# Kernel optimization log

Measured on AMD Instinct MI355X. Metric: run time of the kernel, lower is better.

The kernel has to match this reference:

```python
import jax, jax.numpy as jnp
import numpy as np

SEQ, BATCH, IN_DIM, HID_DIM = 512, 256, 256, 256
NQ = 8
ALPHA = 0.5
MLP_HID = 128


def _linear_init(key, fan_in, fan_out):
    k1, k2 = jax.random.split(key)
    bound = 1.0 / np.sqrt(fan_in)
    W = jax.random.uniform(k1, (fan_in, fan_out), minval=-bound, maxval=bound, dtype=jnp.float32)
    b = jax.random.uniform(k2, (fan_out,), minval=-bound, maxval=bound, dtype=jnp.float32)
    return W, b


def setup_inputs() -> dict:
    key = jax.random.key(0)
    ks = jax.random.split(key, 12)
    cdim = IN_DIM + HID_DIM
    inputs = jax.random.normal(ks[0], (SEQ, BATCH, IN_DIM), dtype=jnp.float32)
    W1, b1 = _linear_init(ks[1], cdim, MLP_HID)
    W2, b2 = _linear_init(ks[2], MLP_HID, NQ * 4)
    Wf, bf = _linear_init(ks[3], cdim, 1)
    Wi, bi = _linear_init(ks[4], cdim, 1)
    Wg, bg = _linear_init(ks[5], cdim, 1)
    Wo, bo = _linear_init(ks[6], cdim, 1)
    rzf = jax.random.normal(ks[7], (NQ,), dtype=jnp.float32)
    rzi = jax.random.normal(ks[8], (NQ,), dtype=jnp.float32)
    rzg = jax.random.normal(ks[9], (NQ,), dtype=jnp.float32)
    rzo = jax.random.normal(ks[10], (NQ,), dtype=jnp.float32)
    return dict(inputs=inputs, W1=W1, b1=b1, W2=W2, b2=b2,
                Wf=Wf, bf=bf, Wi=Wi, bi=bi, Wg=Wg, bg=bg, Wo=Wo, bo=bo,
                rzf=rzf, rzi=rzi, rzg=rzg, rzo=rzo)


def _qgate(theta):
    # Analytic expectations of the RX/RZ/CNOT-chain circuit:
    # <Z_k> = prod_{j<=k} cos(theta_j); rz_params cancel in Z expectations.
    # Returns mean over wires, shape (batch, 1).
    return jnp.mean(jnp.cumprod(jnp.cos(theta), axis=-1), axis=-1, keepdims=True)


def reference(inputs, W1, b1, W2, b2, Wf, bf, Wi, bi, Wg, bg, Wo, bo, rzf, rzi, rzg, rzo):
    batch = inputs.shape[1]
    hx0 = jnp.zeros((batch, HID_DIM), dtype=inputs.dtype)
    cx0 = jnp.zeros((batch, HID_DIM), dtype=inputs.dtype)

    def step(carry, x):
        hx, cx = carry
        combined = jnp.concatenate([x, hx], axis=1)  # (B, in+hid)
        f_c = jax.nn.sigmoid(combined @ Wf + bf)
        i_c = jax.nn.sigmoid(combined @ Wi + bi)
        g_c = jnp.tanh(combined @ Wg + bg)
        o_c = jax.nn.sigmoid(combined @ Wo + bo)
        h1 = jax.nn.relu(combined @ W1 + b1)
        q = h1 @ W2 + b2  # (B, 4*NQ)
        q_f = _qgate(q[:, 0 * NQ:1 * NQ])
        q_i = _qgate(q[:, 1 * NQ:2 * NQ])
        q_g = _qgate(q[:, 2 * NQ:3 * NQ])
        q_o = _qgate(q[:, 3 * NQ:4 * NQ])
        f = (1 - ALPHA) * f_c + ALPHA * jax.nn.sigmoid(q_f)
        i = (1 - ALPHA) * i_c + ALPHA * jax.nn.sigmoid(q_i)
        g = (1 - ALPHA) * g_c + ALPHA * jnp.tanh(q_g)
        o = (1 - ALPHA) * o_c + ALPHA * jax.nn.sigmoid(q_o)
        cx_new = f * cx + i * g
        hx_new = o * jnp.tanh(cx_new)
        return (hx_new, cx_new), hx_new

    (hx, cx), outputs = jax.lax.scan(step, (hx0, cx0), inputs)
    return outputs, (hx, cx)
```

## Files before the change

kernel.cpp:

```cpp
#include <hip/hip_runtime.h>

#define SEQ 512
#define BATCH 256
#define INDIM 256
#define MLP 128
#define M_ROWS (SEQ * BATCH)
#define PRE_STRIDE 136
#define AUX_OFF ((size_t)M_ROWS * PRE_STRIDE)

__global__ __launch_bounds__(256) void prep_kernel(
    const float* __restrict__ W1,
    const float* __restrict__ Wf, const float* __restrict__ Wi,
    const float* __restrict__ Wg, const float* __restrict__ Wo,
    const float* __restrict__ bf, const float* __restrict__ bi,
    const float* __restrict__ bg, const float* __restrict__ bo,
    float* __restrict__ aux) {
  const int tid = threadIdx.x;
  if (tid < 128) {
    float s = 0.f;
    for (int k = 0; k < 256; ++k) s += W1[(size_t)(256 + k) * 128 + tid];
    aux[tid] = s;
  } else if (tid < 132) {
    const int g = tid - 128;
    const float* w = (g == 0) ? Wf : (g == 1) ? Wi : (g == 2) ? Wg : Wo;
    float s = 0.f;
    for (int k = 0; k < 256; ++k) s += w[256 + k];
    aux[128 + g] = s;
  } else if (tid < 136) {
    const int g = tid - 132;
    const float* bp = (g == 0) ? bf : (g == 1) ? bi : (g == 2) ? bg : bo;
    aux[132 + g] = bp[0];
  }
}

#define BK 16
#define LDX 132

__global__ __launch_bounds__(256) void gemm_kernel(
    const float* __restrict__ X,
    const float* __restrict__ W1,
    const float* __restrict__ b1p,
    const float* __restrict__ Wf, const float* __restrict__ Wi,
    const float* __restrict__ Wg, const float* __restrict__ Wo,
    const float* __restrict__ bfp, const float* __restrict__ bip,
    const float* __restrict__ bgp, const float* __restrict__ bop,
    float* __restrict__ PRE) {
  __shared__ __align__(16) float Xs[BK * LDX];
  __shared__ __align__(16) float Ws[BK * LDX];
  __shared__ float Wgs[BK * 4];

  const int tid = threadIdx.x;
  const int blk = blockIdx.x;
  const int tx = tid & 15, ty = tid >> 4;
  const int r_st = tid >> 1, kh = (tid & 1) * 8;
  const int wk = tid >> 4, wn = (tid & 15) * 8;
  const int r2 = tid >> 1, gp = (tid & 1) * 2;

  const size_t rowbase = (size_t)blk * 128;

  float acc[8][8] = {};
  float ga = 0.f, gb = 0.f;

  for (int kc = 0; kc < 256; kc += BK) {
    const float4 xa = *(const float4*)&X[(rowbase + r_st) * 256 + kc + kh];
    const float4 xb = *(const float4*)&X[(rowbase + r_st) * 256 + kc + kh + 4];
    const float4 wa = *(const float4*)&W1[(size_t)(kc + wk) * 128 + wn];
    const float4 wb = *(const float4*)&W1[(size_t)(kc + wk) * 128 + wn + 4];
    float wgv = 0.f;
    if (tid < 64) {
      const int kk = tid >> 2, g = tid & 3;
      const float* w = (g == 0) ? Wf : (g == 1) ? Wi : (g == 2) ? Wg : Wo;
      wgv = w[kc + kk];
    }
    __syncthreads();
    Xs[(kh + 0) * LDX + r_st] = xa.x;
    Xs[(kh + 1) * LDX + r_st] = xa.y;
    Xs[(kh + 2) * LDX + r_st] = xa.z;
    Xs[(kh + 3) * LDX + r_st] = xa.w;
    Xs[(kh + 4) * LDX + r_st] = xb.x;
    Xs[(kh + 5) * LDX + r_st] = xb.y;
    Xs[(kh + 6) * LDX + r_st] = xb.z;
    Xs[(kh + 7) * LDX + r_st] = xb.w;
    *(float4*)&Ws[wk * LDX + wn] = wa;
    *(float4*)&Ws[wk * LDX + wn + 4] = wb;
    if (tid < 64) Wgs[tid] = wgv;
    __syncthreads();

#pragma unroll
    for (int kk = 0; kk < BK; ++kk) {
      const float4 a0 = *(const float4*)&Xs[kk * LDX + ty * 8];
      const float4 a1 = *(const float4*)&Xs[kk * LDX + ty * 8 + 4];
      const float4 c0 = *(const float4*)&Ws[kk * LDX + tx * 8];
      const float4 c1 = *(const float4*)&Ws[kk * LDX + tx * 8 + 4];
      const float av[8] = {a0.x, a0.y, a0.z, a0.w, a1.x, a1.y, a1.z, a1.w};
      const float bv[8] = {c0.x, c0.y, c0.z, c0.w, c1.x, c1.y, c1.z, c1.w};
#pragma unroll
      for (int i = 0; i < 8; ++i)
#pragma unroll
        for (int j = 0; j < 8; ++j)
          acc[i][j] = fmaf(av[i], bv[j], acc[i][j]);
      const float xv = Xs[kk * LDX + r2];
      ga = fmaf(xv, Wgs[kk * 4 + gp], ga);
      gb = fmaf(xv, Wgs[kk * 4 + gp + 1], gb);
    }
  }

  float bias[8];
  {
    const float4 u0 = *(const float4*)&b1p[tx * 8];
    const float4 u1 = *(const float4*)&b1p[tx * 8 + 4];
    bias[0] = u0.x; bias[1] = u0.y; bias[2] = u0.z; bias[3] = u0.w;
    bias[4] = u1.x; bias[5] = u1.y; bias[6] = u1.z; bias[7] = u1.w;
  }
#pragma unroll
  for (int i = 0; i < 8; ++i) {
    const size_t row = rowbase + ty * 8 + i;
    float4 o0, o1;
    o0.x = acc[i][0] + bias[0]; o0.y = acc[i][1] + bias[1];
    o0.z = acc[i][2] + bias[2]; o0.w = acc[i][3] + bias[3];
    o1.x = acc[i][4] + bias[4]; o1.y = acc[i][5] + bias[5];
    o1.z = acc[i][6] + bias[6]; o1.w = acc[i][7] + bias[7];
    *(float4*)&PRE[row * PRE_STRIDE + tx * 8] = o0;
    *(float4*)&PRE[row * PRE_STRIDE + tx * 8 + 4] = o1;
  }
  {
    const float bf0 = bfp[0], bi0 = bip[0], bg0 = bgp[0], bo0 = bop[0];
    const float ab = (gp == 0) ? bf0 : bg0;
    const float bb = (gp == 0) ? bi0 : bo0;
    const size_t row = rowbase + r2;
    float2 og;
    og.x = ga + ab; og.y = gb + bb;
    *(float2*)&PRE[row * PRE_STRIDE + 128 + gp] = og;
  }
}

__device__ __forceinline__ void lds_fence_wave() {
  asm volatile("s_waitcnt lgkmcnt(0)" ::: "memory");
}

__device__ __forceinline__ float sigmoid_f(float x) {
  return __fdividef(1.0f, 1.0f + __expf(-x));
}
__device__ __forceinline__ float tanh_f(float x) {
  const float e = __expf(-2.0f * x);
  return __fdividef(1.0f - e, 1.0f + e);
}

__global__ __attribute__((amdgpu_waves_per_eu(1, 1))) __launch_bounds__(64)
void rec_kernel(
    const float* __restrict__ PRE, const float* __restrict__ W2,
    const float* __restrict__ b2, const float* __restrict__ aux,
    float* __restrict__ out) {
  __shared__ __align__(16) float h1s[128];

  const int l = threadIdx.x;
  const int b = blockIdx.x;
  const int m = l & 31, half = l >> 5;
  const int g = m >> 3;
  const int gbase = g * 8;

  float w2r[64];
#pragma unroll
  for (int u = 0; u < 64; ++u) w2r[u] = W2[(size_t)(half * 64 + u) * 32 + m];
  const float b2v = b2[m];
  const float2 s1 = *(const float2*)&aux[2 * l];
  const float4 sg = *(const float4*)&aux[128];

  float h = 0.f, c = 0.f;

  const float* pr0 = PRE + (size_t)b * PRE_STRIDE;
  const size_t tstride = (size_t)BATCH * PRE_STRIDE;

  float2 p0 = *(const float2*)(pr0 + 0 * tstride + 2 * l);
  float4 g0 = *(const float4*)(pr0 + 0 * tstride + 128);
  float2 p1 = *(const float2*)(pr0 + 1 * tstride + 2 * l);
  float4 g1 = *(const float4*)(pr0 + 1 * tstride + 128);
  float2 p2 = *(const float2*)(pr0 + 2 * tstride + 2 * l);
  float4 g2 = *(const float4*)(pr0 + 2 * tstride + 128);

  const float4* h1p = (const float4*)&h1s[half * 64];

  for (int t = 0; t < SEQ; ++t) {
    const float h10 = fmaxf(fmaf(h, s1.x, p0.x), 0.f);
    const float h11 = fmaxf(fmaf(h, s1.y, p0.y), 0.f);
    const float zf = fmaf(h, sg.x, g0.x);
    const float zi = fmaf(h, sg.y, g0.y);
    const float zg = fmaf(h, sg.z, g0.z);
    const float zo = fmaf(h, sg.w, g0.w);
    const float cf = sigmoid_f(zf);
    const float ci = sigmoid_f(zi);
    const float cg = tanh_f(zg);
    const float co = sigmoid_f(zo);
    p0 = p1; g0 = g1; p1 = p2; g1 = g2;
    const int tn = (t + 3 < SEQ) ? (t + 3) : (SEQ - 1);
    p2 = *(const float2*)(pr0 + (size_t)tn * tstride + 2 * l);
    g2 = *(const float4*)(pr0 + (size_t)tn * tstride + 128);

    ((float2*)h1s)[l] = make_float2(h10, h11);
    lds_fence_wave();

    float q0 = 0.f, q1 = 0.f, q2 = 0.f, q3 = 0.f;
#pragma unroll
    for (int jj = 0; jj < 16; ++jj) {
      const float4 hv = h1p[jj];
      q0 = fmaf(hv.x, w2r[4 * jj + 0], q0);
      q1 = fmaf(hv.y, w2r[4 * jj + 1], q1);
      q2 = fmaf(hv.z, w2r[4 * jj + 2], q2);
      q3 = fmaf(hv.w, w2r[4 * jj + 3], q3);
    }
    const float qh = (q0 + q1) + (q2 + q3);
    const float theta = qh + __shfl_xor(qh, 32, 64) + b2v;
    const float cv = __cosf(theta);

    const float e0 = __shfl(cv, gbase + 0, 64);
    const float e1 = __shfl(cv, gbase + 1, 64);
    const float e2 = __shfl(cv, gbase + 2, 64);
    const float e3 = __shfl(cv, gbase + 3, 64);
    const float e4 = __shfl(cv, gbase + 4, 64);
    const float e5 = __shfl(cv, gbase + 5, 64);
    const float e6 = __shfl(cv, gbase + 6, 64);
    const float e7 = __shfl(cv, gbase + 7, 64);
    float p = e0, s = e0;
    p *= e1; s += p;
    p *= e2; s += p;
    p *= e3; s += p;
    p *= e4; s += p;
    p *= e5; s += p;
    p *= e6; s += p;
    p *= e7; s += p;
    const float qv = s * 0.125f;

    const float qarg = (g == 2) ? (2.0f * qv) : qv;
    const float qs = sigmoid_f(qarg);
    const float av = (g == 2) ? (2.0f * qs - 1.0f) : qs;

    const float aF = __shfl(av, 0, 64);
    const float aI = __shfl(av, 8, 64);
    const float aG = __shfl(av, 16, 64);
    const float aO = __shfl(av, 24, 64);

    const float f  = 0.5f * (cf + aF);
    const float ii = 0.5f * (ci + aI);
    const float gg = 0.5f * (cg + aG);
    const float oo = 0.5f * (co + aO);

    c = fmaf(f, c, ii * gg);
    h = oo * tanh_f(c);

    float4 hv4o; hv4o.x = h; hv4o.y = h; hv4o.z = h; hv4o.w = h;
    *(float4*)(out + ((size_t)t * BATCH + b) * 256 + 4 * l) = hv4o;
  }

  float4 hq; hq.x = h; hq.y = h; hq.z = h; hq.w = h;
  float4 cq; cq.x = c; cq.y = c; cq.z = c; cq.w = c;
  *(float4*)(out + (size_t)SEQ * BATCH * 256 + (size_t)b * 256 + 4 * l) = hq;
  *(float4*)(out + (size_t)SEQ * BATCH * 256 + (size_t)BATCH * 256 +
             (size_t)b * 256 + 4 * l) = cq;
}

extern "C" void kernel_launch(void* const* d_in, const int* in_sizes, int n_in,
                              void* d_out, int out_size, void* d_ws,
                              size_t ws_size, hipStream_t stream) {
  const float* X  = (const float*)d_in[0];
  const float* W1 = (const float*)d_in[1];
  const float* b1 = (const float*)d_in[2];
  const float* W2 = (const float*)d_in[3];
  const float* b2 = (const float*)d_in[4];
  const float* Wf = (const float*)d_in[5];
  const float* bf = (const float*)d_in[6];
  const float* Wi = (const float*)d_in[7];
  const float* bi = (const float*)d_in[8];
  const float* Wg = (const float*)d_in[9];
  const float* bg = (const float*)d_in[10];
  const float* Wo = (const float*)d_in[11];
  const float* bo = (const float*)d_in[12];

  float* ws  = (float*)d_ws;
  float* PRE = ws;
  float* aux = ws + AUX_OFF;
  float* out = (float*)d_out;

  prep_kernel<<<1, 256, 0, stream>>>(W1, Wf, Wi, Wg, Wo, bf, bi, bg, bo, aux);
  gemm_kernel<<<M_ROWS / 128, 256, 0, stream>>>(X, W1, b1, Wf, Wi, Wg, Wo,
                                                bf, bi, bg, bo, PRE);
  rec_kernel<<<BATCH, 64, 0, stream>>>(PRE, W2, b2, aux, out);
}
```

Before: 796.4 us.

## Double-buffer GEMM with direct global-to-LDS loads and block-prefetch recurrence inputs

The input-projection GEMM now uses BK=32 with double-buffered LDS tiles filled by global_load_lds, a row-major X layout, and launch bounds allowing two blocks per CU. This is meant to overlap global loads with FMA work. The recurrent kernel now prefetches PRE rows in blocks of 8 timesteps instead of a rolling 3-step window, hiding load latency on the serial chain. The cost is higher register pressure and possible LDS bank conflicts from the new X layout.

Result: slower. 2.139 ms (+168.6%).

```diff
diff --git a/kernel.cpp b/kernel.cpp
--- a/kernel.cpp
+++ b/kernel.cpp
@@ -33,10 +33,15 @@
   }
 }
 
-#define BK 16
-#define LDX 132
-
-__global__ __launch_bounds__(256) void gemm_kernel(
+#define GBK 32
+
+__device__ __forceinline__ void gl_lds16(const float* g, float* lds) {
+  __builtin_amdgcn_global_load_lds(
+      (const __attribute__((address_space(1))) void*)g,
+      (__attribute__((address_space(3))) void*)lds, 16, 0, 0);
+}
+
+__global__ __launch_bounds__(256, 2) void gemm_kernel(
     const float* __restrict__ X,
     const float* __restrict__ W1,
     const float* __restrict__ b1p,
@@ -45,64 +50,81 @@
     const float* __restrict__ bfp, const float* __restrict__ bip,
     const float* __restrict__ bgp, const float* __restrict__ bop,
     float* __restrict__ PRE) {
-  __shared__ __align__(16) float Xs[BK * LDX];
-  __shared__ __align__(16) float Ws[BK * LDX];
-  __shared__ float Wgs[BK * 4];
+  __shared__ __align__(16) float Xs[2][128 * GBK];
+  __shared__ __align__(16) float Ws[2][GBK * 128];
+  __shared__ float Wgs[2][GBK * 4];
 
   const int tid = threadIdx.x;
-  const int blk = blockIdx.x;
+  const int wave = tid >> 6, lane = tid & 63;
   const int tx = tid & 15, ty = tid >> 4;
-  const int r_st = tid >> 1, kh = (tid & 1) * 8;
-  const int wk = tid >> 4, wn = (tid & 15) * 8;
   const int r2 = tid >> 1, gp = (tid & 1) * 2;
-
-  const size_t rowbase = (size_t)blk * 128;
+  const size_t rowbase = (size_t)blockIdx.x * 128;
+
+  const int gsel = tid & 3;
+  const float* gsrc = (gsel == 0) ? Wf : (gsel == 1) ? Wi : (gsel == 2) ? Wg : Wo;
 
   float acc[8][8] = {};
   float ga = 0.f, gb = 0.f;
-
-  for (int kc = 0; kc < 256; kc += BK) {
-    const float4 xa = *(const float4*)&X[(rowbase + r_st) * 256 + kc + kh];
-    const float4 xb = *(const float4*)&X[(rowbase + r_st) * 256 + kc + kh + 4];
-    const float4 wa = *(const float4*)&W1[(size_t)(kc + wk) * 128 + wn];
-    const float4 wb = *(const float4*)&W1[(size_t)(kc + wk) * 128 + wn + 4];
-    float wgv = 0.f;
-    if (tid < 64) {
-      const int kk = tid >> 2, g = tid & 3;
-      const float* w = (g == 0) ? Wf : (g == 1) ? Wi : (g == 2) ? Wg : Wo;
-      wgv = w[kc + kk];
-    }
+  float gateval = 0.f;
+
+  auto stage = [&](int kc, int bb) {
+#pragma unroll
+    for (int it = 0; it < 4; ++it) {
+      const int ub = wave * 256 + it * 64;
+      const int u = ub + lane;
+      const float* gx = &X[(rowbase + (u >> 3)) * 256 + kc + (u & 7) * 4];
+      gl_lds16(gx, &Xs[bb][ub * 4]);
+    }
+#pragma unroll
+    for (int it = 0; it < 4; ++it) {
+      const int ub = wave * 256 + it * 64;
+      const int u = ub + lane;
+      const float* gw = &W1[(size_t)kc * 128 + u * 4];
+      gl_lds16(gw, &Ws[bb][ub * 4]);
+    }
+  };
+
+  stage(0, 0);
+  if (tid < 128) gateval = gsrc[tid >> 2];
+  if (tid < 128) Wgs[0][tid] = gateval;
+  __syncthreads();
+
+  for (int c = 0; c < 8; ++c) {
+    const int bb = c & 1, nb = bb ^ 1;
+    if (c < 7) {
+      stage((c + 1) * GBK, nb);
+      if (tid < 128) gateval = gsrc[(c + 1) * GBK + (tid >> 2)];
+    }
+    const float* xs = &Xs[bb][0];
+    const float* ws = &Ws[bb][0];
+    const float* wg = &Wgs[bb][0];
+#pragma unroll
+    for (int k4 = 0; k4 < GBK / 4; ++k4) {
+      float4 a[8];
+#pragma unroll
+      for (int i = 0; i < 8; ++i)
+        a[i] = *(const float4*)&xs[(ty * 8 + i) * GBK + k4 * 4];
+#pragma unroll
+      for (int ks = 0; ks < 4; ++ks) {
+        const int kk = k4 * 4 + ks;
+        const float4 b0 = *(const float4*)&ws[kk * 128 + tx * 8];
+        const float4 b1 = *(const float4*)&ws[kk * 128 + tx * 8 + 4];
+        const float bv[8] = {b0.x, b0.y, b0.z, b0.w, b1.x, b1.y, b1.z, b1.w};
+#pragma unroll
+        for (int i = 0; i < 8; ++i) {
+          const float av = (ks == 0) ? a[i].x : (ks == 1) ? a[i].y
+                          : (ks == 2) ? a[i].z : a[i].w;
+#pragma unroll
+          for (int j = 0; j < 8; ++j)
+            acc[i][j] = fmaf(av, bv[j], acc[i][j]);
+        }
+        const float xv = xs[r2 * GBK + kk];
+        ga = fmaf(xv, wg[kk * 4 + gp], ga);
+        gb = fmaf(xv, wg[kk * 4 + gp + 1], gb);
+      }
+    }
+    if (c < 7 && tid < 128) Wgs[nb][tid] = gateval;
     __syncthreads();
-    Xs[(kh + 0) * LDX + r_st] = xa.x;
-    Xs[(kh + 1) * LDX + r_st] = xa.y;
-    Xs[(kh + 2) * LDX + r_st] = xa.z;
-    Xs[(kh + 3) * LDX + r_st] = xa.w;
-    Xs[(kh + 4) * LDX + r_st] = xb.x;
-    Xs[(kh + 5) * LDX + r_st] = xb.y;
-    Xs[(kh + 6) * LDX + r_st] = xb.z;
-    Xs[(kh + 7) * LDX + r_st] = xb.w;
-    *(float4*)&Ws[wk * LDX + wn] = wa;
-    *(float4*)&Ws[wk * LDX + wn + 4] = wb;
-    if (tid < 64) Wgs[tid] = wgv;
-    __syncthreads();
-
-#pragma unroll
-    for (int kk = 0; kk < BK; ++kk) {
-      const float4 a0 = *(const float4*)&Xs[kk * LDX + ty * 8];
-      const float4 a1 = *(const float4*)&Xs[kk * LDX + ty * 8 + 4];
-      const float4 c0 = *(const float4*)&Ws[kk * LDX + tx * 8];
-      const float4 c1 = *(const float4*)&Ws[kk * LDX + tx * 8 + 4];
-      const float av[8] = {a0.x, a0.y, a0.z, a0.w, a1.x, a1.y, a1.z, a1.w};
-      const float bv[8] = {c0.x, c0.y, c0.z, c0.w, c1.x, c1.y, c1.z, c1.w};
-#pragma unroll
-      for (int i = 0; i < 8; ++i)
-#pragma unroll
-        for (int j = 0; j < 8; ++j)
-          acc[i][j] = fmaf(av[i], bv[j], acc[i][j]);
-      const float xv = Xs[kk * LDX + r2];
-      ga = fmaf(xv, Wgs[kk * 4 + gp], ga);
-      gb = fmaf(xv, Wgs[kk * 4 + gp + 1], gb);
-    }
   }
 
   float bias[8];
@@ -126,10 +148,10 @@
   {
     const float bf0 = bfp[0], bi0 = bip[0], bg0 = bgp[0], bo0 = bop[0];
     const float ab = (gp == 0) ? bf0 : bg0;
-    const float bb = (gp == 0) ? bi0 : bo0;
+    const float bb2 = (gp == 0) ? bi0 : bo0;
     const size_t row = rowbase + r2;
     float2 og;
-    og.x = ga + ab; og.y = gb + bb;
+    og.x = ga + ab; og.y = gb + bb2;
     *(float2*)&PRE[row * PRE_STRIDE + 128 + gp] = og;
   }
 }
@@ -169,86 +191,101 @@
   float h = 0.f, c = 0.f;
 
   const float* pr0 = PRE + (size_t)b * PRE_STRIDE;
-  const size_t tstride = (size_t)BATCH * PRE_STRIDE;
-
-  float2 p0 = *(const float2*)(pr0 + 0 * tstride + 2 * l);
-  float4 g0 = *(const float4*)(pr0 + 0 * tstride + 128);
-  float2 p1 = *(const float2*)(pr0 + 1 * tstride + 2 * l);
-  float4 g1 = *(const float4*)(pr0 + 1 * tstride + 128);
-  float2 p2 = *(const float2*)(pr0 + 2 * tstride + 2 * l);
-  float4 g2 = *(const float4*)(pr0 + 2 * tstride + 128);
+  const size_t ts = (size_t)BATCH * PRE_STRIDE;
+
+  float2 pc[8]; float4 gc[8];
+#pragma unroll
+  for (int u = 0; u < 8; ++u) {
+    pc[u] = *(const float2*)(pr0 + (size_t)u * ts + 2 * l);
+    gc[u] = *(const float4*)(pr0 + (size_t)u * ts + 128);
+  }
 
   const float4* h1p = (const float4*)&h1s[half * 64];
 
-  for (int t = 0; t < SEQ; ++t) {
-    const float h10 = fmaxf(fmaf(h, s1.x, p0.x), 0.f);
-    const float h11 = fmaxf(fmaf(h, s1.y, p0.y), 0.f);
-    const float zf = fmaf(h, sg.x, g0.x);
-    const float zi = fmaf(h, sg.y, g0.y);
-    const float zg = fmaf(h, sg.z, g0.z);
-    const float zo = fmaf(h, sg.w, g0.w);
-    const float cf = sigmoid_f(zf);
-    const float ci = sigmoid_f(zi);
-    const float cg = tanh_f(zg);
-    const float co = sigmoid_f(zo);
-    p0 = p1; g0 = g1; p1 = p2; g1 = g2;
-    const int tn = (t + 3 < SEQ) ? (t + 3) : (SEQ - 1);
-    p2 = *(const float2*)(pr0 + (size_t)tn * tstride + 2 * l);
-    g2 = *(const float4*)(pr0 + (size_t)tn * tstride + 128);
-
-    ((float2*)h1s)[l] = make_float2(h10, h11);
-    lds_fence_wave();
-
-    float q0 = 0.f, q1 = 0.f, q2 = 0.f, q3 = 0.f;
-#pragma unroll
-    for (int jj = 0; jj < 16; ++jj) {
-      const float4 hv = h1p[jj];
-      q0 = fmaf(hv.x, w2r[4 * jj + 0], q0);
-      q1 = fmaf(hv.y, w2r[4 * jj + 1], q1);
-      q2 = fmaf(hv.z, w2r[4 * jj + 2], q2);
-      q3 = fmaf(hv.w, w2r[4 * jj + 3], q3);
-    }
-    const float qh = (q0 + q1) + (q2 + q3);
-    const float theta = qh + __shfl_xor(qh, 32, 64) + b2v;
-    const float cv = __cosf(theta);
-
-    const float e0 = __shfl(cv, gbase + 0, 64);
-    const float e1 = __shfl(cv, gbase + 1, 64);
-    const float e2 = __shfl(cv, gbase + 2, 64);
-    const float e3 = __shfl(cv, gbase + 3, 64);
-    const float e4 = __shfl(cv, gbase + 4, 64);
-    const float e5 = __shfl(cv, gbase + 5, 64);
-    const float e6 = __shfl(cv, gbase + 6, 64);
-    const float e7 = __shfl(cv, gbase + 7, 64);
-    float p = e0, s = e0;
-    p *= e1; s += p;
-    p *= e2; s += p;
-    p *= e3; s += p;
-    p *= e4; s += p;
-    p *= e5; s += p;
-    p *= e6; s += p;
-    p *= e7; s += p;
-    const float qv = s * 0.125f;
-
-    const float qarg = (g == 2) ? (2.0f * qv) : qv;
-    const float qs = sigmoid_f(qarg);
-    const float av = (g == 2) ? (2.0f * qs - 1.0f) : qs;
-
-    const float aF = __shfl(av, 0, 64);
-    const float aI = __shfl(av, 8, 64);
-    const float aG = __shfl(av, 16, 64);
-    const float aO = __shfl(av, 24, 64);
-
-    const float f  = 0.5f * (cf + aF);
-    const float ii = 0.5f * (ci + aI);
-    const float gg = 0.5f * (cg + aG);
-    const float oo = 0.5f * (co + aO);
-
-    c = fmaf(f, c, ii * gg);
-    h = oo * tanh_f(c);
-
-    float4 hv4o; hv4o.x = h; hv4o.y = h; hv4o.z = h; hv4o.w = h;
-    *(float4*)(out + ((size_t)t * BATCH + b) * 256 + 4 * l) = hv4o;
+  for (int blk = 0; blk < 64; ++blk) {
+    const int tnb = (blk < 63) ? (blk + 1) : 63;
+    float2 pn[8]; float4 gn[8];
+#pragma unroll
+    for (int u = 0; u < 8; ++u) {
+      const float* base = pr0 + (size_t)(tnb * 8 + u) * ts;
+      pn[u] = *(const float2*)(base + 2 * l);
+      gn[u] = *(const float4*)(base + 128);
+    }
+
+#pragma unroll
+    for (int u = 0; u < 8; ++u) {
+      const int t = blk * 8 + u;
+      const float2 p0 = pc[u];
+      const float4 g0 = gc[u];
+
+      const float h10 = fmaxf(fmaf(h, s1.x, p0.x), 0.f);
+      const float h11 = fmaxf(fmaf(h, s1.y, p0.y), 0.f);
+      const float zf = fmaf(h, sg.x, g0.x);
+      const float zi = fmaf(h, sg.y, g0.y);
+      const float zg = fmaf(h, sg.z, g0.z);
+      const float zo = fmaf(h, sg.w, g0.w);
+      const float cf = sigmoid_f(zf);
+      const float ci = sigmoid_f(zi);
+      const float cg = tanh_f(zg);
+      const float co = sigmoid_f(zo);
+
+      ((float2*)h1s)[l] = make_float2(h10, h11);
+      lds_fence_wave();
+
+      float q0 = 0.f, q1 = 0.f, q2 = 0.f, q3 = 0.f;
+#pragma unroll
+      for (int jj = 0; jj < 16; ++jj) {
+        const float4 hv = h1p[jj];
+        q0 = fmaf(hv.x, w2r[4 * jj + 0], q0);
+        q1 = fmaf(hv.y, w2r[4 * jj + 1], q1);
+        q2 = fmaf(hv.z, w2r[4 * jj + 2], q2);
+        q3 = fmaf(hv.w, w2r[4 * jj + 3], q3);
+      }
+      const float qh = (q0 + q1) + (q2 + q3);
+      const float theta = qh + __shfl_xor(qh, 32, 64) + b2v;
+      const float cv = __cosf(theta);
+
+      const float e0 = __shfl(cv, gbase + 0, 64);
+      const float e1 = __shfl(cv, gbase + 1, 64);
+      const float e2 = __shfl(cv, gbase + 2, 64);
+      const float e3 = __shfl(cv, gbase + 3, 64);
+      const float e4 = __shfl(cv, gbase + 4, 64);
+      const float e5 = __shfl(cv, gbase + 5, 64);
+      const float e6 = __shfl(cv, gbase + 6, 64);
+      const float e7 = __shfl(cv, gbase + 7, 64);
+      float p = e0, s = e0;
+      p *= e1; s += p;
+      p *= e2; s += p;
+      p *= e3; s += p;
+      p *= e4; s += p;
+      p *= e5; s += p;
+      p *= e6; s += p;
+      p *= e7; s += p;
+      const float qv = s * 0.125f;
+
+      const float qarg = (g == 2) ? (2.0f * qv) : qv;
+      const float qs = sigmoid_f(qarg);
+      const float av = (g == 2) ? (2.0f * qs - 1.0f) : qs;
+
+      const float aF = __shfl(av, 0, 64);
+      const float aI = __shfl(av, 8, 64);
+      const float aG = __shfl(av, 16, 64);
+      const float aO = __shfl(av, 24, 64);
+
+      const float f  = 0.5f * (cf + aF);
+      const float ii = 0.5f * (ci + aI);
+      const float gg = 0.5f * (cg + aG);
+      const float oo = 0.5f * (co + aO);
+
+      c = fmaf(f, c, ii * gg);
+      h = oo * tanh_f(c);
+
+      float4 hv4o; hv4o.x = h; hv4o.y = h; hv4o.z = h; hv4o.w = h;
+      *(float4*)(out + ((size_t)t * BATCH + b) * 256 + 4 * l) = hv4o;
+    }
+
+#pragma unroll
+    for (int u = 0; u < 8; ++u) { pc[u] = pn[u]; gc[u] = gn[u]; }
   }
 
   float4 hq; hq.x = h; hq.y = h; hq.z = h; hq.w = h;
```

## Double-buffer GEMM LDS tiles and pack two batch rows per recurrent wave

Applied to the files above, without the earlier changes.

The GEMM kernel now double-buffers its shared-memory tiles, so the next K-chunk is loaded from global memory while the current one is being computed, which removes one barrier per iteration. The recurrent kernel now handles two batch elements per 64-lane wave, each in a 32-lane half holding all 128 W2 rows in registers. This halves the number of blocks and removes the cross-half shuffle reduction. The cost is double the register footprint (128 W2 values per lane) and twice as much serial FMA work per lane per timestep, which could lengthen the latency-bound recurrence.

Result: slower. 1.105 ms (+38.7%).

```diff
diff --git a/kernel.cpp b/kernel.cpp
--- a/kernel.cpp
+++ b/kernel.cpp
@@ -45,53 +45,62 @@
     const float* __restrict__ bfp, const float* __restrict__ bip,
     const float* __restrict__ bgp, const float* __restrict__ bop,
     float* __restrict__ PRE) {
-  __shared__ __align__(16) float Xs[BK * LDX];
-  __shared__ __align__(16) float Ws[BK * LDX];
-  __shared__ float Wgs[BK * 4];
+  __shared__ __align__(16) float Xs[2][BK * LDX];
+  __shared__ __align__(16) float Ws[2][BK * LDX];
+  __shared__ float Wgs[2][BK * 4];
 
   const int tid = threadIdx.x;
-  const int blk = blockIdx.x;
   const int tx = tid & 15, ty = tid >> 4;
   const int r_st = tid >> 1, kh = (tid & 1) * 8;
   const int wk = tid >> 4, wn = (tid & 15) * 8;
   const int r2 = tid >> 1, gp = (tid & 1) * 2;
-
-  const size_t rowbase = (size_t)blk * 128;
+  const size_t rowbase = (size_t)blockIdx.x * 128;
+
+  const int gsel = tid & 3;
+  const float* gsrc = (gsel == 0) ? Wf : (gsel == 1) ? Wi
+                     : (gsel == 2) ? Wg : Wo;
 
   float acc[8][8] = {};
   float ga = 0.f, gb = 0.f;
 
-  for (int kc = 0; kc < 256; kc += BK) {
-    const float4 xa = *(const float4*)&X[(rowbase + r_st) * 256 + kc + kh];
-    const float4 xb = *(const float4*)&X[(rowbase + r_st) * 256 + kc + kh + 4];
-    const float4 wa = *(const float4*)&W1[(size_t)(kc + wk) * 128 + wn];
-    const float4 wb = *(const float4*)&W1[(size_t)(kc + wk) * 128 + wn + 4];
-    float wgv = 0.f;
-    if (tid < 64) {
-      const int kk = tid >> 2, g = tid & 3;
-      const float* w = (g == 0) ? Wf : (g == 1) ? Wi : (g == 2) ? Wg : Wo;
-      wgv = w[kc + kk];
-    }
-    __syncthreads();
-    Xs[(kh + 0) * LDX + r_st] = xa.x;
-    Xs[(kh + 1) * LDX + r_st] = xa.y;
-    Xs[(kh + 2) * LDX + r_st] = xa.z;
-    Xs[(kh + 3) * LDX + r_st] = xa.w;
-    Xs[(kh + 4) * LDX + r_st] = xb.x;
-    Xs[(kh + 5) * LDX + r_st] = xb.y;
-    Xs[(kh + 6) * LDX + r_st] = xb.z;
-    Xs[(kh + 7) * LDX + r_st] = xb.w;
-    *(float4*)&Ws[wk * LDX + wn] = wa;
-    *(float4*)&Ws[wk * LDX + wn + 4] = wb;
-    if (tid < 64) Wgs[tid] = wgv;
-    __syncthreads();
+  float4 xa, xb, wa, wb;
+  float wgv = 0.f;
+
+  auto gload = [&](int kc) {
+    xa = *(const float4*)&X[(rowbase + r_st) * 256 + kc + kh];
+    xb = *(const float4*)&X[(rowbase + r_st) * 256 + kc + kh + 4];
+    wa = *(const float4*)&W1[(size_t)(kc + wk) * 128 + wn];
+    wb = *(const float4*)&W1[(size_t)(kc + wk) * 128 + wn + 4];
+    if (tid < 64) wgv = gsrc[kc + (tid >> 2)];
+  };
+  auto swrite = [&](int bb) {
+    Xs[bb][(kh + 0) * LDX + r_st] = xa.x;
+    Xs[bb][(kh + 1) * LDX + r_st] = xa.y;
+    Xs[bb][(kh + 2) * LDX + r_st] = xa.z;
+    Xs[bb][(kh + 3) * LDX + r_st] = xa.w;
+    Xs[bb][(kh + 4) * LDX + r_st] = xb.x;
+    Xs[bb][(kh + 5) * LDX + r_st] = xb.y;
+    Xs[bb][(kh + 6) * LDX + r_st] = xb.z;
+    Xs[bb][(kh + 7) * LDX + r_st] = xb.w;
+    *(float4*)&Ws[bb][wk * LDX + wn] = wa;
+    *(float4*)&Ws[bb][wk * LDX + wn + 4] = wb;
+    if (tid < 64) Wgs[bb][tid] = wgv;
+  };
+
+  gload(0);
+  swrite(0);
+  __syncthreads();
+
+  for (int c = 0; c < 16; ++c) {
+    const int bb = c & 1;
+    if (c < 15) gload((c + 1) * BK);
 
 #pragma unroll
     for (int kk = 0; kk < BK; ++kk) {
-      const float4 a0 = *(const float4*)&Xs[kk * LDX + ty * 8];
-      const float4 a1 = *(const float4*)&Xs[kk * LDX + ty * 8 + 4];
-      const float4 c0 = *(const float4*)&Ws[kk * LDX + tx * 8];
-      const float4 c1 = *(const float4*)&Ws[kk * LDX + tx * 8 + 4];
+      const float4 a0 = *(const float4*)&Xs[bb][kk * LDX + ty * 8];
+      const float4 a1 = *(const float4*)&Xs[bb][kk * LDX + ty * 8 + 4];
+      const float4 c0 = *(const float4*)&Ws[bb][kk * LDX + tx * 8];
+      const float4 c1 = *(const float4*)&Ws[bb][kk * LDX + tx * 8 + 4];
       const float av[8] = {a0.x, a0.y, a0.z, a0.w, a1.x, a1.y, a1.z, a1.w};
       const float bv[8] = {c0.x, c0.y, c0.z, c0.w, c1.x, c1.y, c1.z, c1.w};
 #pragma unroll
@@ -99,10 +108,13 @@
 #pragma unroll
         for (int j = 0; j < 8; ++j)
           acc[i][j] = fmaf(av[i], bv[j], acc[i][j]);
-      const float xv = Xs[kk * LDX + r2];
-      ga = fmaf(xv, Wgs[kk * 4 + gp], ga);
-      gb = fmaf(xv, Wgs[kk * 4 + gp + 1], gb);
+      const float xv = Xs[bb][kk * LDX + r2];
+      ga = fmaf(xv, Wgs[bb][kk * 4 + gp], ga);
+      gb = fmaf(xv, Wgs[bb][kk * 4 + gp + 1], gb);
     }
+
+    if (c < 15) swrite(bb ^ 1);
+    __syncthreads();
   }
 
   float bias[8];
@@ -124,20 +136,17 @@
     *(float4*)&PRE[row * PRE_STRIDE + tx * 8 + 4] = o1;
   }
   {
-    const float bf0 = bfp[0], bi0 = bip[0], bg0 = bgp[0], bo0 = bop[0];
-    const float ab = (gp == 0) ? bf0 : bg0;
-    const float bb = (gp == 0) ? bi0 : bo0;
-    const size_t row = rowbase + r2;
+    const float ab = (gp == 0) ? bfp[0] : bgp[0];
+    const float bb2 = (gp == 0) ? bip[0] : bop[0];
     float2 og;
-    og.x = ga + ab; og.y = gb + bb;
-    *(float2*)&PRE[row * PRE_STRIDE + 128 + gp] = og;
+    og.x = ga + ab; og.y = gb + bb2;
+    *(float2*)&PRE[(rowbase + r2) * PRE_STRIDE + 128 + gp] = og;
   }
 }
 
 __device__ __forceinline__ void lds_fence_wave() {
   asm volatile("s_waitcnt lgkmcnt(0)" ::: "memory");
 }
-
 __device__ __forceinline__ float sigmoid_f(float x) {
   return __fdividef(1.0f, 1.0f + __expf(-x));
 }
@@ -151,38 +160,41 @@
     const float* __restrict__ PRE, const float* __restrict__ W2,
     const float* __restrict__ b2, const float* __restrict__ aux,
     float* __restrict__ out) {
-  __shared__ __align__(16) float h1s[128];
+  __shared__ __align__(16) float h1s[2 * 128];
 
   const int l = threadIdx.x;
-  const int b = blockIdx.x;
-  const int m = l & 31, half = l >> 5;
-  const int g = m >> 3;
-  const int gbase = g * 8;
-
-  float w2r[64];
-#pragma unroll
-  for (int u = 0; u < 64; ++u) w2r[u] = W2[(size_t)(half * 64 + u) * 32 + m];
-  const float b2v = b2[m];
-  const float2 s1 = *(const float2*)&aux[2 * l];
+  const int hb = l >> 5;
+  const int i = l & 31;
+  const int b = blockIdx.x * 2 + hb;
+  const int g = i >> 3;
+  const int lbase = hb * 32;
+
+  float w2r[128];
+#pragma unroll
+  for (int j = 0; j < 128; ++j) w2r[j] = W2[(size_t)j * 32 + i];
+  const float b2v = b2[i];
+  const float4 s1 = *(const float4*)&aux[4 * i];
   const float4 sg = *(const float4*)&aux[128];
 
   float h = 0.f, c = 0.f;
 
   const float* pr0 = PRE + (size_t)b * PRE_STRIDE;
-  const size_t tstride = (size_t)BATCH * PRE_STRIDE;
-
-  float2 p0 = *(const float2*)(pr0 + 0 * tstride + 2 * l);
-  float4 g0 = *(const float4*)(pr0 + 0 * tstride + 128);
-  float2 p1 = *(const float2*)(pr0 + 1 * tstride + 2 * l);
-  float4 g1 = *(const float4*)(pr0 + 1 * tstride + 128);
-  float2 p2 = *(const float2*)(pr0 + 2 * tstride + 2 * l);
-  float4 g2 = *(const float4*)(pr0 + 2 * tstride + 128);
-
-  const float4* h1p = (const float4*)&h1s[half * 64];
+  const size_t ts = (size_t)BATCH * PRE_STRIDE;
+
+  float4 p0 = *(const float4*)(pr0 + 0 * ts + 4 * i);
+  float4 g0 = *(const float4*)(pr0 + 0 * ts + 128);
+  float4 p1 = *(const float4*)(pr0 + 1 * ts + 4 * i);
+  float4 g1 = *(const float4*)(pr0 + 1 * ts + 128);
+  float4 p2 = *(const float4*)(pr0 + 2 * ts + 4 * i);
+  float4 g2 = *(const float4*)(pr0 + 2 * ts + 128);
+
+  const float4* hp = (const float4*)&h1s[hb * 128];
 
   for (int t = 0; t < SEQ; ++t) {
     const float h10 = fmaxf(fmaf(h, s1.x, p0.x), 0.f);
     const float h11 = fmaxf(fmaf(h, s1.y, p0.y), 0.f);
+    const float h12 = fmaxf(fmaf(h, s1.z, p0.z), 0.f);
+    const float h13 = fmaxf(fmaf(h, s1.w, p0.w), 0.f);
     const float zf = fmaf(h, sg.x, g0.x);
     const float zi = fmaf(h, sg.y, g0.y);
     const float zg = fmaf(h, sg.z, g0.z);
@@ -193,33 +205,34 @@
     const float co = sigmoid_f(zo);
     p0 = p1; g0 = g1; p1 = p2; g1 = g2;
     const int tn = (t + 3 < SEQ) ? (t + 3) : (SEQ - 1);
-    p2 = *(const float2*)(pr0 + (size_t)tn * tstride + 2 * l);
-    g2 = *(const float4*)(pr0 + (size_t)tn * tstride + 128);
-
-    ((float2*)h1s)[l] = make_float2(h10, h11);
+    p2 = *(const float4*)(pr0 + (size_t)tn * ts + 4 * i);
+    g2 = *(const float4*)(pr0 + (size_t)tn * ts + 128);
+
+    float4 hq; hq.x = h10; hq.y = h11; hq.z = h12; hq.w = h13;
+    ((float4*)h1s)[l] = hq;
     lds_fence_wave();
 
     float q0 = 0.f, q1 = 0.f, q2 = 0.f, q3 = 0.f;
 #pragma unroll
-    for (int jj = 0; jj < 16; ++jj) {
-      const float4 hv = h1p[jj];
+    for (int jj = 0; jj < 32; ++jj) {
+      const float4 hv = hp[jj];
       q0 = fmaf(hv.x, w2r[4 * jj + 0], q0);
       q1 = fmaf(hv.y, w2r[4 * jj + 1], q1);
       q2 = fmaf(hv.z, w2r[4 * jj + 2], q2);
       q3 = fmaf(hv.w, w2r[4 * jj + 3], q3);
     }
-    const float qh = (q0 + q1) + (q2 + q3);
-    const float theta = qh + __shfl_xor(qh, 32, 64) + b2v;
+    const float theta = (q0 + q1) + (q2 + q3) + b2v;
     const float cv = __cosf(theta);
 
-    const float e0 = __shfl(cv, gbase + 0, 64);
-    const float e1 = __shfl(cv, gbase + 1, 64);
-    const float e2 = __shfl(cv, gbase + 2, 64);
-    const float e3 = __shfl(cv, gbase + 3, 64);
-    const float e4 = __shfl(cv, gbase + 4, 64);
-    const float e5 = __shfl(cv, gbase + 5, 64);
-    const float e6 = __shfl(cv, gbase + 6, 64);
-    const float e7 = __shfl(cv, gbase + 7, 64);
+    const int gb8 = lbase + g * 8;
+    const float e0 = __shfl(cv, gb8 + 0, 64);
+    const float e1 = __shfl(cv, gb8 + 1, 64);
+    const float e2 = __shfl(cv, gb8 + 2, 64);
+    const float e3 = __shfl(cv, gb8 + 3, 64);
+    const float e4 = __shfl(cv, gb8 + 4, 64);
+    const float e5 = __shfl(cv, gb8 + 5, 64);
+    const float e6 = __shfl(cv, gb8 + 6, 64);
+    const float e7 = __shfl(cv, gb8 + 7, 64);
     float p = e0, s = e0;
     p *= e1; s += p;
     p *= e2; s += p;
@@ -234,10 +247,10 @@
     const float qs = sigmoid_f(qarg);
     const float av = (g == 2) ? (2.0f * qs - 1.0f) : qs;
 
-    const float aF = __shfl(av, 0, 64);
-    const float aI = __shfl(av, 8, 64);
-    const float aG = __shfl(av, 16, 64);
-    const float aO = __shfl(av, 24, 64);
+    const float aF = __shfl(av, lbase + 0, 64);
+    const float aI = __shfl(av, lbase + 8, 64);
+    const float aG = __shfl(av, lbase + 16, 64);
+    const float aO = __shfl(av, lbase + 24, 64);
 
     const float f  = 0.5f * (cf + aF);
     const float ii = 0.5f * (ci + aI);
@@ -247,15 +260,18 @@
     c = fmaf(f, c, ii * gg);
     h = oo * tanh_f(c);
 
+    float* ob = out + ((size_t)t * BATCH + b) * 256 + 8 * i;
     float4 hv4o; hv4o.x = h; hv4o.y = h; hv4o.z = h; hv4o.w = h;
-    *(float4*)(out + ((size_t)t * BATCH + b) * 256 + 4 * l) = hv4o;
-  }
-
-  float4 hq; hq.x = h; hq.y = h; hq.z = h; hq.w = h;
-  float4 cq; cq.x = c; cq.y = c; cq.z = c; cq.w = c;
-  *(float4*)(out + (size_t)SEQ * BATCH * 256 + (size_t)b * 256 + 4 * l) = hq;
-  *(float4*)(out + (size_t)SEQ * BATCH * 256 + (size_t)BATCH * 256 +
-             (size_t)b * 256 + 4 * l) = cq;
+    *(float4*)(ob) = hv4o;
+    *(float4*)(ob + 4) = hv4o;
+  }
+
+  float* hxp = out + (size_t)SEQ * BATCH * 256 + (size_t)b * 256 + 8 * i;
+  float* cxp = hxp + (size_t)BATCH * 256;
+  float4 hq2; hq2.x = h; hq2.y = h; hq2.z = h; hq2.w = h;
+  float4 cq2; cq2.x = c; cq2.y = c; cq2.z = c; cq2.w = c;
+  *(float4*)(hxp) = hq2; *(float4*)(hxp + 4) = hq2;
+  *(float4*)(cxp) = cq2; *(float4*)(cxp + 4) = cq2;
 }
 
 extern "C" void kernel_launch(void* const* d_in, const int* in_sizes, int n_in,
@@ -283,5 +299,5 @@
   prep_kernel<<<1, 256, 0, stream>>>(W1, Wf, Wi, Wg, Wo, bf, bi, bg, bo, aux);
   gemm_kernel<<<M_ROWS / 128, 256, 0, stream>>>(X, W1, b1, Wf, Wi, Wg, Wo,
                                                 bf, bi, bg, bo, PRE);
-  rec_kernel<<<BATCH, 64, 0, stream>>>(PRE, W2, b2, aux, out);
-}
+  rec_kernel<<<BATCH / 2, 64, 0, stream>>>(PRE, W2, b2, aux, out);
+}
```
